# Kernel tuning notes

Measured on AMD Instinct MI355X. Metric: run time of the kernel, lower is better.

The kernel has to match this reference:

```python
import jax, jax.numpy as jnp
import numpy as np
import math

DIM = 768
HEADS = 12
HEAD_DIM = DIM // HEADS


def setup_inputs() -> dict:
    key = jax.random.key(0)
    ks = jax.random.split(key, 9)
    s = 1.0 / math.sqrt(DIM)
    x = jax.random.normal(ks[0], (8, 4096, DIM), dtype=jnp.float32)
    Wq = jax.random.normal(ks[1], (DIM, DIM), dtype=jnp.float32) * s
    bq = jnp.zeros((DIM,), dtype=jnp.float32)
    Wk = jax.random.normal(ks[2], (DIM, DIM), dtype=jnp.float32) * s
    bk = jnp.zeros((DIM,), dtype=jnp.float32)
    Wv = jax.random.normal(ks[3], (DIM, DIM), dtype=jnp.float32) * s
    bv = jnp.zeros((DIM,), dtype=jnp.float32)
    Wp = jax.random.normal(ks[4], (DIM, DIM), dtype=jnp.float32) * s
    bp = jnp.zeros((DIM,), dtype=jnp.float32)
    return {"x": x, "Wq": Wq, "bq": bq, "Wk": Wk, "bk": bk,
            "Wv": Wv, "bv": bv, "Wp": Wp, "bp": bp}


def reference(x, Wq, bq, Wk, bk, Wv, bv, Wp, bp):
    B, N, C = x.shape
    H, D = HEADS, HEAD_DIM
    # torch Linear: y = x @ W.T + b
    q = (x @ Wq.T + bq).reshape(B, N, H, D).transpose(0, 2, 1, 3)  # [B,H,N,D]
    k = (x @ Wk.T + bk).reshape(B, N, H, D).transpose(0, 2, 1, 3)
    v = (x @ Wv.T + bv).reshape(B, N, H, D).transpose(0, 2, 1, 3)
    q = jax.nn.softmax(q, axis=-1)   # softmax over head_dim
    k = jax.nn.softmax(k, axis=-2)   # softmax over sequence
    kv = jnp.einsum('bhnd,bhne->bhde', k, v) / math.sqrt(D)  # [B,H,D,D]
    out = jnp.einsum('bhnd,bhde->bhne', q, kv)               # [B,H,N,D]
    out = out.transpose(0, 2, 1, 3).reshape(B, N, C)
    return out @ Wp.T + bp
```

## Files before the change

kernel.cpp:

```cpp
#include <hip/hip_runtime.h>
#include <hip/hip_bf16.h>


#define AS1 __attribute__((address_space(1)))
#define AS3 __attribute__((address_space(3)))

typedef __attribute__((ext_vector_type(8))) short    s16x8;
typedef __attribute__((ext_vector_type(4))) float    f32x4;
typedef __attribute__((ext_vector_type(8))) _Float16 f16x8;
typedef __attribute__((ext_vector_type(4))) unsigned short u16x4;

__device__ __forceinline__ unsigned short f2bf(float f) {
  union { float f; unsigned u; } v; v.f = f;
  unsigned r = v.u + 0x7FFFu + ((v.u >> 16) & 1u);
  return (unsigned short)(r >> 16);
}

__global__ __launch_bounds__(256) void prep(const float* __restrict__ x,
                                            const float* __restrict__ Wq, const float* __restrict__ Wk,
                                            const float* __restrict__ Wv,
                                            const float* __restrict__ bq, const float* __restrict__ bk,
                                            const float* __restrict__ bv,
                                            unsigned short* __restrict__ x_bf,
                                            unsigned short* __restrict__ wqkv_bf,
                                            float* __restrict__ bqkv) {
  const int XB = 2304;
  if ((int)blockIdx.x >= XB) {
    int j = (blockIdx.x - XB) * 256 + threadIdx.x;
    if (j < 768) bqkv[j] = bq[j];
    else if (j < 1536) bqkv[j] = bk[j - 768];
    else if (j < 2304) bqkv[j] = bv[j - 1536];
    return;
  }
  const int n8x = 3145728, n8w = 73728;
  const int stride = XB * 256;
  for (int i = blockIdx.x * 256 + threadIdx.x; i < n8x + 3 * n8w; i += stride) {
    const float* s; unsigned short* d;
    if (i < n8x) { s = x + (size_t)i * 8; d = x_bf + (size_t)i * 8; }
    else {
      int wi = i - n8x, w = wi / n8w, off = wi - w * n8w;
      const float* ws_ = (w == 0) ? Wq : (w == 1) ? Wk : Wv;
      s = ws_ + (size_t)off * 8; d = wqkv_bf + (size_t)wi * 8;
    }
    f32x4 a = ((const f32x4*)s)[0], b = ((const f32x4*)s)[1];
    u16x4 lo, hi;
    lo[0] = f2bf(a[0]); lo[1] = f2bf(a[1]); lo[2] = f2bf(a[2]); lo[3] = f2bf(a[3]);
    hi[0] = f2bf(b[0]); hi[1] = f2bf(b[1]); hi[2] = f2bf(b[2]); hi[3] = f2bf(b[3]);
    ((u16x4*)d)[0] = lo; ((u16x4*)d)[1] = hi;
  }
}

template <int MODE, int BMBLK>
__global__ __launch_bounds__(512, 2) void gemm256(const unsigned short* __restrict__ A,
                                                  const unsigned short* __restrict__ Bm,
                                                  const float* __restrict__ bias,
                                                  void* out0, void* out1, void* out2,
                                                  int N, int K, int nb, int batchedB) {
  constexpr int BM = BMBLK * 128;
  __shared__ unsigned short As[2][BM * 64];
  __shared__ unsigned short Bs[2][256 * 64];
  const int tid = threadIdx.x, lane = tid & 63, wid = tid >> 6;
  const int wr = wid >> 2, wc = wid & 3;
  const int cpx = gridDim.x >> 3;
  const int logical = (blockIdx.x & 7) * cpx + (blockIdx.x >> 3);
  const int m0 = (logical / nb) * BM, n0 = (logical % nb) * 256;
  const unsigned short* Bp = Bm + (batchedB ? ((size_t)(m0 >> 12) * 589824) : 0);

  f32x4 acc[BMBLK * 4][4] = {};
  const int srcc8 = ((lane & 7) ^ (lane >> 3)) * 8;

  auto stageA = [&](int buf, int which, int k0) {
    if constexpr (BMBLK == 2) {
#pragma unroll
      for (int half = 0; half < 2; ++half) {
        int row = half * 128 + which * 64 + (tid >> 3);
        __builtin_amdgcn_global_load_lds(
            (const AS1 void*)(A + (size_t)(m0 + row) * K + k0 + srcc8),
            (AS3 void*)(&As[buf][row * 64 + (tid & 7) * 8]), 16, 0, 0);
      }
    } else {
#pragma unroll
      for (int j = 0; j < 2; ++j) {
        int row = j * 64 + (tid >> 3);
        __builtin_amdgcn_global_load_lds(
            (const AS1 void*)(A + (size_t)(m0 + row) * K + k0 + srcc8),
            (AS3 void*)(&As[buf][row * 64 + (tid & 7) * 8]), 16, 0, 0);
      }
    }
  };
  auto stageB = [&](int buf, int which, int k0) {
#pragma unroll
    for (int j = 0; j < 2; ++j) {
      int idx = tid + j * 512;
      int half = idx >> 9, sub = (idx >> 8) & 1;
      int row = half * 128 + sub * 64 + which * 32 + ((idx & 255) >> 3);
      __builtin_amdgcn_global_load_lds(
          (const AS1 void*)(Bp + (size_t)(n0 + row) * K + k0 + srcc8),
          (AS3 void*)(&Bs[buf][row * 64 + (idx & 7) * 8]), 16, 0, 0);
    }
  };

  const int r15 = lane & 15, hi8 = (lane >> 4) * 8, sw = (lane & 7) * 8;
  s16x8 af[4][2], bf[4][2];
  auto readA = [&](int buf, int grp) {
    const unsigned short* base = &As[buf][(wr * (BM / 2) + grp * 64) * 64];
#pragma unroll
    for (int i = 0; i < 4; ++i) {
      int lrow = i * 16 + r15;
#pragma unroll
      for (int kk = 0; kk < 2; ++kk)
        af[i][kk] = *(const s16x8*)(base + lrow * 64 + ((kk * 32 + hi8) ^ sw));
    }
  };
  auto readB = [&](int buf, int grp) {
    const unsigned short* base = &Bs[buf][(wc >> 1) * 128 * 64];
#pragma unroll
    for (int jj = 0; jj < 2; ++jj) {
      int j = grp * 2 + jj;
      int lrow = (wc & 1) * 64 + j * 16 + r15;
#pragma unroll
      for (int kk = 0; kk < 2; ++kk)
        bf[j][kk] = *(const s16x8*)(base + lrow * 64 + ((kk * 32 + hi8) ^ sw));
    }
  };

#define MFMA16(MI0, J0)                                                             \
  __builtin_amdgcn_s_setprio(1);                                                    \
  _Pragma("unroll") for (int kk = 0; kk < 2; ++kk)                                  \
  _Pragma("unroll") for (int i = 0; i < 4; ++i)                                     \
  _Pragma("unroll") for (int jj = 0; jj < 2; ++jj)                                  \
    acc[(MI0) + i][(J0) + jj] = __builtin_amdgcn_mfma_f32_16x16x32_bf16(            \
        af[i][kk], bf[(J0) + jj][kk], acc[(MI0) + i][(J0) + jj], 0, 0, 0);          \
  __builtin_amdgcn_s_setprio(0);

  const int nt = K >> 6;
  if constexpr (BMBLK == 2) {
    stageA(0, 0, 0);  stageA(0, 1, 0);  stageB(0, 0, 0);  stageB(0, 1, 0);
    stageA(1, 0, 64); stageA(1, 1, 64); stageB(1, 0, 64); stageB(1, 1, 64);
    asm volatile("s_waitcnt vmcnt(8)" ::: "memory");
  } else {
    stageA(0, 0, 0);  stageB(0, 0, 0);  stageB(0, 1, 0);
    stageA(1, 0, 64); stageB(1, 0, 64); stageB(1, 1, 64);
    asm volatile("s_waitcnt vmcnt(6)" ::: "memory");
  }
  __builtin_amdgcn_s_barrier();

  for (int s = 0; s < nt; ++s) {
    const int buf = s & 1;
    const int k2 = (s + 2) << 6;
    const bool pf = (s + 2) < nt;
    if constexpr (BMBLK == 2) {
      readA(buf, 0); readB(buf, 0);
      asm volatile("" ::: "memory");
      __builtin_amdgcn_s_barrier();
      asm volatile("s_waitcnt lgkmcnt(0)" ::: "memory");
      MFMA16(0, 0)
      asm volatile("" ::: "memory");
      __builtin_amdgcn_s_barrier();
      readB(buf, 1);
      if (pf) { stageA(buf, 0, k2); stageB(buf, 0, k2); }
      asm volatile("" ::: "memory");
      __builtin_amdgcn_s_barrier();
      asm volatile("s_waitcnt lgkmcnt(0)" ::: "memory");
      MFMA16(0, 2)
      asm volatile("" ::: "memory");
      __builtin_amdgcn_s_barrier();
      readA(buf, 1);
      if (pf) stageB(buf, 1, k2);
      asm volatile("" ::: "memory");
      __builtin_amdgcn_s_barrier();
      asm volatile("s_waitcnt lgkmcnt(0)" ::: "memory");
      MFMA16(4, 2)
      asm volatile("" ::: "memory");
      __builtin_amdgcn_s_barrier();
      if (pf) stageA(buf, 1, k2);
      MFMA16(4, 0)
      if (pf)              asm volatile("s_waitcnt vmcnt(8)" ::: "memory");
      else if (s + 1 < nt) asm volatile("s_waitcnt vmcnt(0)" ::: "memory");
      __builtin_amdgcn_s_barrier();
    } else {
      readA(buf, 0); readB(buf, 0); readB(buf, 1);
      asm volatile("" ::: "memory");
      __builtin_amdgcn_s_barrier();
      asm volatile("s_waitcnt lgkmcnt(0)" ::: "memory");
      MFMA16(0, 0)
      asm volatile("" ::: "memory");
      __builtin_amdgcn_s_barrier();
      if (pf) { stageA(buf, 0, k2); stageB(buf, 0, k2); stageB(buf, 1, k2); }
      MFMA16(0, 2)
      if (pf)              asm volatile("s_waitcnt vmcnt(6)" ::: "memory");
      else if (s + 1 < nt) asm volatile("s_waitcnt vmcnt(0)" ::: "memory");
      __builtin_amdgcn_s_barrier();
    }
  }

  const int g = lane >> 4, c15 = lane & 15;
  float bj[4];
#pragma unroll
  for (int j = 0; j < 4; ++j) bj[j] = bias[n0 + wc * 64 + j * 16 + c15];

  if (MODE == 0) {
    float* out = (float*)out0;
#pragma unroll
    for (int mi = 0; mi < BMBLK * 4; ++mi)
#pragma unroll
      for (int j = 0; j < 4; ++j) {
        int gr = m0 + wr * (BM / 2) + mi * 16 + g * 4;
        int gc = n0 + wc * 64 + j * 16 + c15;
#pragma unroll
        for (int r = 0; r < 4; ++r)
          out[(size_t)(gr + r) * N + gc] = acc[mi][j][r] + bj[j];
      }
  } else {
    if (n0 < 768) {
      unsigned short* qsm = (unsigned short*)out0;
      const int cbase = n0 + wc * 64;
#pragma unroll
      for (int mi = 0; mi < BMBLK * 4; ++mi) {
#pragma unroll
        for (int r = 0; r < 4; ++r) {
          int gr = m0 + wr * (BM / 2) + mi * 16 + g * 4 + r;
          float v[4];
#pragma unroll
          for (int j = 0; j < 4; ++j) v[j] = acc[mi][j][r] + bj[j];
          float mx = fmaxf(fmaxf(v[0], v[1]), fmaxf(v[2], v[3]));
#pragma unroll
          for (int st = 1; st < 16; st <<= 1) mx = fmaxf(mx, __shfl_xor(mx, st));
          float p[4], sm = 0.f;
#pragma unroll
          for (int j = 0; j < 4; ++j) { p[j] = __expf(v[j] - mx); sm += p[j]; }
#pragma unroll
          for (int st = 1; st < 16; st <<= 1) sm += __shfl_xor(sm, st);
          float inv = 1.0f / sm;
#pragma unroll
          for (int j = 0; j < 4; ++j)
            qsm[(size_t)gr * 768 + cbase + j * 16 + c15] = f2bf(p[j] * inv);
        }
      }
    } else {
      _Float16* dst = (n0 < 1536) ? (_Float16*)out1 : (_Float16*)out2;
      const int cbase = (n0 < 1536 ? n0 - 768 : n0 - 1536) + wc * 64;
#pragma unroll
      for (int mi = 0; mi < BMBLK * 4; ++mi)
#pragma unroll
        for (int j = 0; j < 4; ++j) {
          int gr = m0 + wr * (BM / 2) + mi * 16 + g * 4;
          int cc = cbase + j * 16 + c15;
#pragma unroll
          for (int r = 0; r < 4; ++r)
            dst[(size_t)(gr + r) * 768 + cc] = (_Float16)(acc[mi][j][r] + bj[j]);
        }
    }
  }
#undef MFMA16
}

__global__ __launch_bounds__(256) void kv_partial(const _Float16* __restrict__ kh,
                                                  const _Float16* __restrict__ vh,
                                                  float* __restrict__ kv_raw,
                                                  float* __restrict__ z_raw) {
  const int bh = blockIdx.x, b = bh / 12, h = bh % 12;
  const int split = blockIdx.y;
  __shared__ float ek_s[64][68];
  __shared__ float v_s[64][68];
  const int t = threadIdx.x;
  const int d0 = (t >> 4) * 4, e0 = (t & 15) * 4;
  const int zd = t & 63, zq = t >> 6;
  float acc[4][4] = {};
  float zp = 0.f;
  const size_t base = (size_t)b * 4096 * 768 + h * 64;

  for (int nc = 0; nc < 8; ++nc) {
    int n0 = split * 512 + nc * 64;
#pragma unroll
    for (int j = 0; j < 2; ++j) {
      int vi = t + j * 256;
      int row = vi >> 3, c8 = (vi & 7) * 8;
      size_t gp = base + (size_t)(n0 + row) * 768 + c8;
      f16x8 k8 = *(const f16x8*)(kh + gp);
      f16x8 v8 = *(const f16x8*)(vh + gp);
      f32x4 e0v, e1v, v0v, v1v;
#pragma unroll
      for (int u = 0; u < 4; ++u) {
        e0v[u] = __expf((float)k8[u]); e1v[u] = __expf((float)k8[4 + u]);
        v0v[u] = (float)v8[u];         v1v[u] = (float)v8[4 + u];
      }
      *(f32x4*)&ek_s[row][c8] = e0v; *(f32x4*)&ek_s[row][c8 + 4] = e1v;
      *(f32x4*)&v_s[row][c8]  = v0v; *(f32x4*)&v_s[row][c8 + 4]  = v1v;
    }
    __syncthreads();
#pragma unroll 4
    for (int r = 0; r < 16; ++r) zp += ek_s[zq * 16 + r][zd];
#pragma unroll 8
    for (int n = 0; n < 64; ++n) {
      f32x4 ekv = *(const f32x4*)&ek_s[n][d0];
      f32x4 vv  = *(const f32x4*)&v_s[n][e0];
#pragma unroll
      for (int i = 0; i < 4; ++i)
#pragma unroll
        for (int j = 0; j < 4; ++j)
          acc[i][j] += ekv[i] * vv[j];
    }
    __syncthreads();
  }
  float* kvp = kv_raw + (size_t)bh * 4096;
#pragma unroll
  for (int i = 0; i < 4; ++i)
#pragma unroll
    for (int j = 0; j < 4; ++j)
      atomicAdd(&kvp[(d0 + i) * 64 + e0 + j], acc[i][j]);
  atomicAdd(&z_raw[bh * 64 + zd], zp);
}

__global__ __launch_bounds__(256) void weff_build(const float* __restrict__ kv_raw,
                                                  const float* __restrict__ z_raw,
                                                  const float* __restrict__ Wp,
                                                  unsigned short* __restrict__ weffT) {
  const int c0 = blockIdx.x * 64, h = blockIdx.y, b = blockIdx.z;
  const int bh = b * 12 + h;
  __shared__ float kvn[64][65];
  const int t = threadIdx.x;
#pragma unroll
  for (int i = 0; i < 16; ++i) {
    int idx = t + i * 256;
    int d = idx >> 6;
    kvn[d][idx & 63] = kv_raw[(size_t)bh * 4096 + idx] / (z_raw[bh * 64 + d] * 8.0f);
  }
  __syncthreads();
  const int c = c0 + (t >> 2);
  const int d0 = (t & 3) * 16;
  const float* wrow = Wp + (size_t)c * 768 + h * 64;
  float acc[16] = {};
#pragma unroll 8
  for (int e = 0; e < 64; ++e) {
    float w = wrow[e];
#pragma unroll
    for (int dd = 0; dd < 16; ++dd) acc[dd] += w * kvn[d0 + dd][e];
  }
  unsigned short* orow = weffT + (size_t)b * 589824 + (size_t)c * 768 + h * 64 + d0;
#pragma unroll
  for (int dd = 0; dd < 16; ++dd) orow[dd] = f2bf(acc[dd]);
}

extern "C" void kernel_launch(void* const* d_in, const int* in_sizes, int n_in,
                              void* d_out, int out_size, void* d_ws, size_t ws_size,
                              hipStream_t stream) {
  const float* x  = (const float*)d_in[0];
  const float* Wq = (const float*)d_in[1];
  const float* bq = (const float*)d_in[2];
  const float* Wk = (const float*)d_in[3];
  const float* bk = (const float*)d_in[4];
  const float* Wv = (const float*)d_in[5];
  const float* bv = (const float*)d_in[6];
  const float* Wp = (const float*)d_in[7];
  const float* bp = (const float*)d_in[8];

  const size_t MT = 32768;
  const size_t XE = MT * 768;
  const size_t WE = 768 * 768;

  unsigned short* x_bf    = (unsigned short*)d_ws;
  unsigned short* wqkv_bf = x_bf + XE;
  unsigned short* q_sm    = wqkv_bf + 3 * WE;
  _Float16* k_h = (_Float16*)(q_sm + XE);
  _Float16* v_h = k_h + XE;
  unsigned short* weffT = (unsigned short*)(v_h + XE);
  float* bqkv   = (float*)(weffT + 8 * WE);
  float* kv_raw = bqkv + 2304;
  float* z_raw  = kv_raw + 96 * 4096;

  prep<<<2313, 256, 0, stream>>>(x, Wq, Wk, Wv, bq, bk, bv, x_bf, wqkv_bf, bqkv);
  hipMemsetAsync(kv_raw, 0, (96 * 4096 + 96 * 64) * sizeof(float), stream);

  gemm256<1, 2><<<1152, 512, 0, stream>>>(x_bf, wqkv_bf, bqkv, q_sm, k_h, v_h, 2304, 768, 9, 0);

  kv_partial<<<dim3(96, 8), 256, 0, stream>>>(k_h, v_h, kv_raw, z_raw);
  weff_build<<<dim3(12, 12, 8), 256, 0, stream>>>(kv_raw, z_raw, Wp, weffT);

  gemm256<0, 1><<<768, 512, 0, stream>>>(q_sm, weffT, bp, d_out, nullptr, nullptr, 768, 768, 3, 1);
}
```

Before: 356.3 us.

## Load GEMM B operand directly from global into registers, drop B LDS staging

The GEMM no longer stages the weight tile (B) through shared memory. Each wave instead loads its B fragments straight from global memory into registers every k-step, and only A keeps double-buffered LDS staging. The finely interleaved barrier/prefetch schedule is replaced by a simple loop: load B, prefetch next A, compute, then wait for all loads and barrier. This halves LDS use and removes the B LDS writes and reads. In exchange, B is fetched redundantly by the two wave rows, global loads now sit on the critical path with less overlap, and the full vmcnt(0) wait each iteration serializes memory and compute.

Result: slower. 456.0 us (+28.0%).

```diff
diff --git a/kernel.cpp b/kernel.cpp
--- a/kernel.cpp
+++ b/kernel.cpp
@@ -57,8 +57,9 @@
                                                   void* out0, void* out1, void* out2,
                                                   int N, int K, int nb, int batchedB) {
   constexpr int BM = BMBLK * 128;
+  constexpr int MI = BMBLK * 4;
+  constexpr int NSTG = 2 * BMBLK;
   __shared__ unsigned short As[2][BM * 64];
-  __shared__ unsigned short Bs[2][256 * 64];
   const int tid = threadIdx.x, lane = tid & 63, wid = tid >> 6;
   const int wr = wid >> 2, wc = wid & 3;
   const int cpx = gridDim.x >> 3;
@@ -66,132 +67,69 @@
   const int m0 = (logical / nb) * BM, n0 = (logical % nb) * 256;
   const unsigned short* Bp = Bm + (batchedB ? ((size_t)(m0 >> 12) * 589824) : 0);
 
-  f32x4 acc[BMBLK * 4][4] = {};
+  f32x4 acc[MI][4] = {};
   const int srcc8 = ((lane & 7) ^ (lane >> 3)) * 8;
-
-  auto stageA = [&](int buf, int which, int k0) {
-    if constexpr (BMBLK == 2) {
-#pragma unroll
-      for (int half = 0; half < 2; ++half) {
-        int row = half * 128 + which * 64 + (tid >> 3);
-        __builtin_amdgcn_global_load_lds(
-            (const AS1 void*)(A + (size_t)(m0 + row) * K + k0 + srcc8),
-            (AS3 void*)(&As[buf][row * 64 + (tid & 7) * 8]), 16, 0, 0);
-      }
-    } else {
-#pragma unroll
-      for (int j = 0; j < 2; ++j) {
-        int row = j * 64 + (tid >> 3);
-        __builtin_amdgcn_global_load_lds(
-            (const AS1 void*)(A + (size_t)(m0 + row) * K + k0 + srcc8),
-            (AS3 void*)(&As[buf][row * 64 + (tid & 7) * 8]), 16, 0, 0);
-      }
+  const int r15 = lane & 15, hi8 = (lane >> 4) * 8, sw = (lane & 7) * 8;
+
+  auto stageA = [&](int buf, int k0) {
+#pragma unroll
+    for (int j = 0; j < NSTG; ++j) {
+      int row = j * 64 + (tid >> 3);
+      __builtin_amdgcn_global_load_lds(
+          (const AS1 void*)(A + (size_t)(m0 + row) * K + k0 + srcc8),
+          (AS3 void*)(&As[buf][row * 64 + (tid & 7) * 8]), 16, 0, 0);
     }
   };
-  auto stageB = [&](int buf, int which, int k0) {
-#pragma unroll
-    for (int j = 0; j < 2; ++j) {
-      int idx = tid + j * 512;
-      int half = idx >> 9, sub = (idx >> 8) & 1;
-      int row = half * 128 + sub * 64 + which * 32 + ((idx & 255) >> 3);
-      __builtin_amdgcn_global_load_lds(
-          (const AS1 void*)(Bp + (size_t)(n0 + row) * K + k0 + srcc8),
-          (AS3 void*)(&Bs[buf][row * 64 + (idx & 7) * 8]), 16, 0, 0);
-    }
+
+  const unsigned short* Bw = Bp + (size_t)(n0 + wc * 64 + r15) * K + hi8;
+  s16x8 bf[4][2];
+  auto loadB = [&](int k0) {
+#pragma unroll
+    for (int j = 0; j < 4; ++j)
+#pragma unroll
+      for (int kk = 0; kk < 2; ++kk)
+        bf[j][kk] = *(const s16x8*)(Bw + (size_t)j * 16 * K + k0 + kk * 32);
   };
 
-  const int r15 = lane & 15, hi8 = (lane >> 4) * 8, sw = (lane & 7) * 8;
-  s16x8 af[4][2], bf[4][2];
+  s16x8 af[4][2];
   auto readA = [&](int buf, int grp) {
     const unsigned short* base = &As[buf][(wr * (BM / 2) + grp * 64) * 64];
 #pragma unroll
-    for (int i = 0; i < 4; ++i) {
-      int lrow = i * 16 + r15;
+    for (int i = 0; i < 4; ++i)
 #pragma unroll
       for (int kk = 0; kk < 2; ++kk)
-        af[i][kk] = *(const s16x8*)(base + lrow * 64 + ((kk * 32 + hi8) ^ sw));
-    }
+        af[i][kk] = *(const s16x8*)(base + (i * 16 + r15) * 64 + ((kk * 32 + hi8) ^ sw));
   };
-  auto readB = [&](int buf, int grp) {
-    const unsigned short* base = &Bs[buf][(wc >> 1) * 128 * 64];
-#pragma unroll
-    for (int jj = 0; jj < 2; ++jj) {
-      int j = grp * 2 + jj;
-      int lrow = (wc & 1) * 64 + j * 16 + r15;
-#pragma unroll
-      for (int kk = 0; kk < 2; ++kk)
-        bf[j][kk] = *(const s16x8*)(base + lrow * 64 + ((kk * 32 + hi8) ^ sw));
-    }
+  auto mfma32 = [&](int mi0) {
+    __builtin_amdgcn_s_setprio(1);
+#pragma unroll
+    for (int i = 0; i < 4; ++i)
+#pragma unroll
+      for (int j = 0; j < 4; ++j)
+#pragma unroll
+        for (int kk = 0; kk < 2; ++kk)
+          acc[mi0 + i][j] = __builtin_amdgcn_mfma_f32_16x16x32_bf16(
+              af[i][kk], bf[j][kk], acc[mi0 + i][j], 0, 0, 0);
+    __builtin_amdgcn_s_setprio(0);
   };
 
-#define MFMA16(MI0, J0)                                                             \
-  __builtin_amdgcn_s_setprio(1);                                                    \
-  _Pragma("unroll") for (int kk = 0; kk < 2; ++kk)                                  \
-  _Pragma("unroll") for (int i = 0; i < 4; ++i)                                     \
-  _Pragma("unroll") for (int jj = 0; jj < 2; ++jj)                                  \
-    acc[(MI0) + i][(J0) + jj] = __builtin_amdgcn_mfma_f32_16x16x32_bf16(            \
-        af[i][kk], bf[(J0) + jj][kk], acc[(MI0) + i][(J0) + jj], 0, 0, 0);          \
-  __builtin_amdgcn_s_setprio(0);
-
   const int nt = K >> 6;
-  if constexpr (BMBLK == 2) {
-    stageA(0, 0, 0);  stageA(0, 1, 0);  stageB(0, 0, 0);  stageB(0, 1, 0);
-    stageA(1, 0, 64); stageA(1, 1, 64); stageB(1, 0, 64); stageB(1, 1, 64);
-    asm volatile("s_waitcnt vmcnt(8)" ::: "memory");
-  } else {
-    stageA(0, 0, 0);  stageB(0, 0, 0);  stageB(0, 1, 0);
-    stageA(1, 0, 64); stageB(1, 0, 64); stageB(1, 1, 64);
-    asm volatile("s_waitcnt vmcnt(6)" ::: "memory");
-  }
+  stageA(0, 0);
+  asm volatile("s_waitcnt vmcnt(0)" ::: "memory");
   __builtin_amdgcn_s_barrier();
 
-  for (int s = 0; s < nt; ++s) {
-    const int buf = s & 1;
-    const int k2 = (s + 2) << 6;
-    const bool pf = (s + 2) < nt;
+  for (int t = 0; t < nt; ++t) {
+    const int buf = t & 1;
+    loadB(t << 6);
+    if (t + 1 < nt) stageA(buf ^ 1, (t + 1) << 6);
+    readA(buf, 0);
+    mfma32(0);
     if constexpr (BMBLK == 2) {
-      readA(buf, 0); readB(buf, 0);
-      asm volatile("" ::: "memory");
-      __builtin_amdgcn_s_barrier();
-      asm volatile("s_waitcnt lgkmcnt(0)" ::: "memory");
-      MFMA16(0, 0)
-      asm volatile("" ::: "memory");
-      __builtin_amdgcn_s_barrier();
-      readB(buf, 1);
-      if (pf) { stageA(buf, 0, k2); stageB(buf, 0, k2); }
-      asm volatile("" ::: "memory");
-      __builtin_amdgcn_s_barrier();
-      asm volatile("s_waitcnt lgkmcnt(0)" ::: "memory");
-      MFMA16(0, 2)
-      asm volatile("" ::: "memory");
-      __builtin_amdgcn_s_barrier();
       readA(buf, 1);
-      if (pf) stageB(buf, 1, k2);
-      asm volatile("" ::: "memory");
-      __builtin_amdgcn_s_barrier();
-      asm volatile("s_waitcnt lgkmcnt(0)" ::: "memory");
-      MFMA16(4, 2)
-      asm volatile("" ::: "memory");
-      __builtin_amdgcn_s_barrier();
-      if (pf) stageA(buf, 1, k2);
-      MFMA16(4, 0)
-      if (pf)              asm volatile("s_waitcnt vmcnt(8)" ::: "memory");
-      else if (s + 1 < nt) asm volatile("s_waitcnt vmcnt(0)" ::: "memory");
-      __builtin_amdgcn_s_barrier();
-    } else {
-      readA(buf, 0); readB(buf, 0); readB(buf, 1);
-      asm volatile("" ::: "memory");
-      __builtin_amdgcn_s_barrier();
-      asm volatile("s_waitcnt lgkmcnt(0)" ::: "memory");
-      MFMA16(0, 0)
-      asm volatile("" ::: "memory");
-      __builtin_amdgcn_s_barrier();
-      if (pf) { stageA(buf, 0, k2); stageB(buf, 0, k2); stageB(buf, 1, k2); }
-      MFMA16(0, 2)
-      if (pf)              asm volatile("s_waitcnt vmcnt(6)" ::: "memory");
-      else if (s + 1 < nt) asm volatile("s_waitcnt vmcnt(0)" ::: "memory");
-      __builtin_amdgcn_s_barrier();
-    }
+      mfma32(4);
+    }
+    asm volatile("s_waitcnt vmcnt(0)" ::: "memory");
+    __builtin_amdgcn_s_barrier();
   }
 
   const int g = lane >> 4, c15 = lane & 15;
@@ -202,7 +140,7 @@
   if (MODE == 0) {
     float* out = (float*)out0;
 #pragma unroll
-    for (int mi = 0; mi < BMBLK * 4; ++mi)
+    for (int mi = 0; mi < MI; ++mi)
 #pragma unroll
       for (int j = 0; j < 4; ++j) {
         int gr = m0 + wr * (BM / 2) + mi * 16 + g * 4;
@@ -216,7 +154,7 @@
       unsigned short* qsm = (unsigned short*)out0;
       const int cbase = n0 + wc * 64;
 #pragma unroll
-      for (int mi = 0; mi < BMBLK * 4; ++mi) {
+      for (int mi = 0; mi < MI; ++mi) {
 #pragma unroll
         for (int r = 0; r < 4; ++r) {
           int gr = m0 + wr * (BM / 2) + mi * 16 + g * 4 + r;
@@ -241,7 +179,7 @@
       _Float16* dst = (n0 < 1536) ? (_Float16*)out1 : (_Float16*)out2;
       const int cbase = (n0 < 1536 ? n0 - 768 : n0 - 1536) + wc * 64;
 #pragma unroll
-      for (int mi = 0; mi < BMBLK * 4; ++mi)
+      for (int mi = 0; mi < MI; ++mi)
 #pragma unroll
         for (int j = 0; j < 4; ++j) {
           int gr = m0 + wr * (BM / 2) + mi * 16 + g * 4;
@@ -252,7 +190,6 @@
         }
     }
   }
-#undef MFMA16
 }
 
 __global__ __launch_bounds__(256) void kv_partial(const _Float16* __restrict__ kh,
```

## Switch GEMM to 32x32x16 MFMA tiles and fold memset into prep kernel

Applied to the files above, without the earlier changes.

Changes both GEMM instantiations from 16x16x32 bf16 MFMA to 32x32x16 bf16 MFMA. Fragment loads, accumulator layout and all epilogues (bias, q softmax over 64 columns, fp16 stores) are rewritten for the new 32-row output mapping. The aim is fewer MFMA issues and LDS fragment reads per tile. It also drops the separate hipMemsetAsync and zeroes kv_raw/z_raw inside the tail blocks of the prep kernel, removing one launch. The softmax epilogue now shuffles across 32 lanes, and the strided per-element stores may hurt coalescing.

New measurement: 381.5 us. +7.1%, slower.

```diff
diff --git a/kernel.cpp b/kernel.cpp
--- a/kernel.cpp
+++ b/kernel.cpp
@@ -7,7 +7,9 @@
 
 typedef __attribute__((ext_vector_type(8))) short    s16x8;
 typedef __attribute__((ext_vector_type(4))) float    f32x4;
+typedef __attribute__((ext_vector_type(16))) float   f32x16;
 typedef __attribute__((ext_vector_type(8))) _Float16 f16x8;
+typedef __attribute__((ext_vector_type(4))) _Float16 f16x4;
 typedef __attribute__((ext_vector_type(4))) unsigned short u16x4;
 
 __device__ __forceinline__ unsigned short f2bf(float f) {
@@ -23,13 +25,16 @@
                                             const float* __restrict__ bv,
                                             unsigned short* __restrict__ x_bf,
                                             unsigned short* __restrict__ wqkv_bf,
-                                            float* __restrict__ bqkv) {
+                                            float* __restrict__ bqkv,
+                                            float* __restrict__ kvz) {
   const int XB = 2304;
   if ((int)blockIdx.x >= XB) {
     int j = (blockIdx.x - XB) * 256 + threadIdx.x;
     if (j < 768) bqkv[j] = bq[j];
     else if (j < 1536) bqkv[j] = bk[j - 768];
     else if (j < 2304) bqkv[j] = bv[j - 1536];
+    const int NZ = 96 * 4096 + 96 * 64;
+    for (int i = (blockIdx.x - XB) * 256 + threadIdx.x; i < NZ; i += 9 * 256) kvz[i] = 0.f;
     return;
   }
   const int n8x = 3145728, n8w = 73728;
@@ -56,7 +61,9 @@
                                                   const float* __restrict__ bias,
                                                   void* out0, void* out1, void* out2,
                                                   int N, int K, int nb, int batchedB) {
-  constexpr int BM = BMBLK * 128;
+  constexpr int BM  = BMBLK * 128;
+  constexpr int MIH = BMBLK;
+  constexpr int MIF = BMBLK * 2;
   __shared__ unsigned short As[2][BM * 64];
   __shared__ unsigned short Bs[2][256 * 64];
   const int tid = threadIdx.x, lane = tid & 63, wid = tid >> 6;
@@ -66,8 +73,9 @@
   const int m0 = (logical / nb) * BM, n0 = (logical % nb) * 256;
   const unsigned short* Bp = Bm + (batchedB ? ((size_t)(m0 >> 12) * 589824) : 0);
 
-  f32x4 acc[BMBLK * 4][4] = {};
+  f32x16 acc[MIF][2] = {};
   const int srcc8 = ((lane & 7) ^ (lane >> 3)) * 8;
+  const int l31 = lane & 31, g8 = (lane >> 5) * 8, sw = (lane & 7) * 8;
 
   auto stageA = [&](int buf, int which, int k0) {
     if constexpr (BMBLK == 2) {
@@ -100,38 +108,33 @@
     }
   };
 
-  const int r15 = lane & 15, hi8 = (lane >> 4) * 8, sw = (lane & 7) * 8;
-  s16x8 af[4][2], bf[4][2];
-  auto readA = [&](int buf, int grp) {
-    const unsigned short* base = &As[buf][(wr * (BM / 2) + grp * 64) * 64];
-#pragma unroll
-    for (int i = 0; i < 4; ++i) {
-      int lrow = i * 16 + r15;
-#pragma unroll
-      for (int kk = 0; kk < 2; ++kk)
-        af[i][kk] = *(const s16x8*)(base + lrow * 64 + ((kk * 32 + hi8) ^ sw));
-    }
-  };
-  auto readB = [&](int buf, int grp) {
+  s16x8 af[2][4], bf[2][4];
+  auto readA = [&](int buf, int h) {
+    const unsigned short* base = &As[buf][(wr * (BM / 2) + h * (BM / 4)) * 64];
+#pragma unroll
+    for (int i = 0; i < MIH; ++i)
+#pragma unroll
+      for (int ks = 0; ks < 4; ++ks)
+        af[BMBLK == 2 ? i : h][ks] =
+            *(const s16x8*)(base + (i * 32 + l31) * 64 + ((ks * 16 + g8) ^ sw));
+  };
+  auto readB = [&](int buf, int q) {
     const unsigned short* base = &Bs[buf][(wc >> 1) * 128 * 64];
-#pragma unroll
-    for (int jj = 0; jj < 2; ++jj) {
-      int j = grp * 2 + jj;
-      int lrow = (wc & 1) * 64 + j * 16 + r15;
-#pragma unroll
-      for (int kk = 0; kk < 2; ++kk)
-        bf[j][kk] = *(const s16x8*)(base + lrow * 64 + ((kk * 32 + hi8) ^ sw));
-    }
-  };
-
-#define MFMA16(MI0, J0)                                                             \
-  __builtin_amdgcn_s_setprio(1);                                                    \
-  _Pragma("unroll") for (int kk = 0; kk < 2; ++kk)                                  \
-  _Pragma("unroll") for (int i = 0; i < 4; ++i)                                     \
-  _Pragma("unroll") for (int jj = 0; jj < 2; ++jj)                                  \
-    acc[(MI0) + i][(J0) + jj] = __builtin_amdgcn_mfma_f32_16x16x32_bf16(            \
-        af[i][kk], bf[(J0) + jj][kk], acc[(MI0) + i][(J0) + jj], 0, 0, 0);          \
-  __builtin_amdgcn_s_setprio(0);
+    int lrow = (wc & 1) * 64 + q * 32 + l31;
+#pragma unroll
+    for (int ks = 0; ks < 4; ++ks)
+      bf[q][ks] = *(const s16x8*)(base + lrow * 64 + ((ks * 16 + g8) ^ sw));
+  };
+  auto mfmaQ = [&](int h, int q) {
+    __builtin_amdgcn_s_setprio(1);
+#pragma unroll
+    for (int ks = 0; ks < 4; ++ks)
+#pragma unroll
+      for (int i = 0; i < MIH; ++i)
+        acc[h * MIH + i][q] = __builtin_amdgcn_mfma_f32_32x32x16_bf16(
+            af[BMBLK == 2 ? i : h][ks], bf[q][ks], acc[h * MIH + i][q], 0, 0, 0);
+    __builtin_amdgcn_s_setprio(0);
+  };
 
   const int nt = K >> 6;
   if constexpr (BMBLK == 2) {
@@ -154,7 +157,7 @@
       asm volatile("" ::: "memory");
       __builtin_amdgcn_s_barrier();
       asm volatile("s_waitcnt lgkmcnt(0)" ::: "memory");
-      MFMA16(0, 0)
+      mfmaQ(0, 0);
       asm volatile("" ::: "memory");
       __builtin_amdgcn_s_barrier();
       readB(buf, 1);
@@ -162,7 +165,7 @@
       asm volatile("" ::: "memory");
       __builtin_amdgcn_s_barrier();
       asm volatile("s_waitcnt lgkmcnt(0)" ::: "memory");
-      MFMA16(0, 2)
+      mfmaQ(0, 1);
       asm volatile("" ::: "memory");
       __builtin_amdgcn_s_barrier();
       readA(buf, 1);
@@ -170,89 +173,90 @@
       asm volatile("" ::: "memory");
       __builtin_amdgcn_s_barrier();
       asm volatile("s_waitcnt lgkmcnt(0)" ::: "memory");
-      MFMA16(4, 2)
+      mfmaQ(1, 1);
       asm volatile("" ::: "memory");
       __builtin_amdgcn_s_barrier();
       if (pf) stageA(buf, 1, k2);
-      MFMA16(4, 0)
+      mfmaQ(1, 0);
       if (pf)              asm volatile("s_waitcnt vmcnt(8)" ::: "memory");
       else if (s + 1 < nt) asm volatile("s_waitcnt vmcnt(0)" ::: "memory");
       __builtin_amdgcn_s_barrier();
     } else {
-      readA(buf, 0); readB(buf, 0); readB(buf, 1);
+      readA(buf, 0); readA(buf, 1); readB(buf, 0); readB(buf, 1);
       asm volatile("" ::: "memory");
       __builtin_amdgcn_s_barrier();
       asm volatile("s_waitcnt lgkmcnt(0)" ::: "memory");
-      MFMA16(0, 0)
+      mfmaQ(0, 0); mfmaQ(1, 0);
       asm volatile("" ::: "memory");
       __builtin_amdgcn_s_barrier();
       if (pf) { stageA(buf, 0, k2); stageB(buf, 0, k2); stageB(buf, 1, k2); }
-      MFMA16(0, 2)
+      mfmaQ(0, 1); mfmaQ(1, 1);
       if (pf)              asm volatile("s_waitcnt vmcnt(6)" ::: "memory");
       else if (s + 1 < nt) asm volatile("s_waitcnt vmcnt(0)" ::: "memory");
       __builtin_amdgcn_s_barrier();
     }
   }
 
-  const int g = lane >> 4, c15 = lane & 15;
-  float bj[4];
-#pragma unroll
-  for (int j = 0; j < 4; ++j) bj[j] = bias[n0 + wc * 64 + j * 16 + c15];
+  const int grp = lane >> 5;
+  float bj[2];
+#pragma unroll
+  for (int q = 0; q < 2; ++q) bj[q] = bias[n0 + wc * 64 + q * 32 + l31];
 
   if (MODE == 0) {
     float* out = (float*)out0;
 #pragma unroll
-    for (int mi = 0; mi < BMBLK * 4; ++mi)
-#pragma unroll
-      for (int j = 0; j < 4; ++j) {
-        int gr = m0 + wr * (BM / 2) + mi * 16 + g * 4;
-        int gc = n0 + wc * 64 + j * 16 + c15;
-#pragma unroll
-        for (int r = 0; r < 4; ++r)
-          out[(size_t)(gr + r) * N + gc] = acc[mi][j][r] + bj[j];
+    for (int mi = 0; mi < MIF; ++mi)
+#pragma unroll
+      for (int q = 0; q < 2; ++q) {
+        int gc = n0 + wc * 64 + q * 32 + l31;
+#pragma unroll
+        for (int r = 0; r < 16; ++r) {
+          int rr = (r & 3) + 8 * (r >> 2) + 4 * grp;
+          int gr = m0 + wr * (BM / 2) + mi * 32 + rr;
+          out[(size_t)gr * N + gc] = acc[mi][q][r] + bj[q];
+        }
       }
   } else {
     if (n0 < 768) {
       unsigned short* qsm = (unsigned short*)out0;
       const int cbase = n0 + wc * 64;
 #pragma unroll
-      for (int mi = 0; mi < BMBLK * 4; ++mi) {
-#pragma unroll
-        for (int r = 0; r < 4; ++r) {
-          int gr = m0 + wr * (BM / 2) + mi * 16 + g * 4 + r;
-          float v[4];
-#pragma unroll
-          for (int j = 0; j < 4; ++j) v[j] = acc[mi][j][r] + bj[j];
-          float mx = fmaxf(fmaxf(v[0], v[1]), fmaxf(v[2], v[3]));
-#pragma unroll
-          for (int st = 1; st < 16; st <<= 1) mx = fmaxf(mx, __shfl_xor(mx, st));
-          float p[4], sm = 0.f;
-#pragma unroll
-          for (int j = 0; j < 4; ++j) { p[j] = __expf(v[j] - mx); sm += p[j]; }
-#pragma unroll
-          for (int st = 1; st < 16; st <<= 1) sm += __shfl_xor(sm, st);
+      for (int mi = 0; mi < MIF; ++mi) {
+#pragma unroll
+        for (int r = 0; r < 16; ++r) {
+          int rr = (r & 3) + 8 * (r >> 2) + 4 * grp;
+          int gr = m0 + wr * (BM / 2) + mi * 32 + rr;
+          float v0 = acc[mi][0][r] + bj[0];
+          float v1 = acc[mi][1][r] + bj[1];
+          float mx = fmaxf(v0, v1);
+#pragma unroll
+          for (int st = 1; st < 32; st <<= 1) mx = fmaxf(mx, __shfl_xor(mx, st));
+          float p0 = __expf(v0 - mx), p1 = __expf(v1 - mx);
+          float sm = p0 + p1;
+#pragma unroll
+          for (int st = 1; st < 32; st <<= 1) sm += __shfl_xor(sm, st);
           float inv = 1.0f / sm;
-#pragma unroll
-          for (int j = 0; j < 4; ++j)
-            qsm[(size_t)gr * 768 + cbase + j * 16 + c15] = f2bf(p[j] * inv);
+          qsm[(size_t)gr * 768 + cbase + l31]      = f2bf(p0 * inv);
+          qsm[(size_t)gr * 768 + cbase + 32 + l31] = f2bf(p1 * inv);
         }
       }
     } else {
       _Float16* dst = (n0 < 1536) ? (_Float16*)out1 : (_Float16*)out2;
       const int cbase = (n0 < 1536 ? n0 - 768 : n0 - 1536) + wc * 64;
 #pragma unroll
-      for (int mi = 0; mi < BMBLK * 4; ++mi)
-#pragma unroll
-        for (int j = 0; j < 4; ++j) {
-          int gr = m0 + wr * (BM / 2) + mi * 16 + g * 4;
-          int cc = cbase + j * 16 + c15;
-#pragma unroll
-          for (int r = 0; r < 4; ++r)
-            dst[(size_t)(gr + r) * 768 + cc] = (_Float16)(acc[mi][j][r] + bj[j]);
+      for (int mi = 0; mi < MIF; ++mi)
+#pragma unroll
+        for (int q = 0; q < 2; ++q) {
+          int cc = cbase + q * 32 + l31;
+#pragma unroll
+          for (int r = 0; r < 16; ++r) {
+            int rr = (r & 3) + 8 * (r >> 2) + 4 * grp;
+            int gr = m0 + wr * (BM / 2) + mi * 32 + rr;
+            dst[(size_t)gr * 768 + cc] = (_Float16)(acc[mi][q][r] + bj[q]);
+          }
         }
     }
   }
-#undef MFMA16
 }
 
 __global__ __launch_bounds__(256) void kv_partial(const _Float16* __restrict__ kh,
@@ -369,8 +373,7 @@
   float* kv_raw = bqkv + 2304;
   float* z_raw  = kv_raw + 96 * 4096;
 
-  prep<<<2313, 256, 0, stream>>>(x, Wq, Wk, Wv, bq, bk, bv, x_bf, wqkv_bf, bqkv);
-  hipMemsetAsync(kv_raw, 0, (96 * 4096 + 96 * 64) * sizeof(float), stream);
+  prep<<<2313, 256, 0, stream>>>(x, Wq, Wk, Wv, bq, bk, bv, x_bf, wqkv_bf, bqkv, kv_raw);
 
   gemm256<1, 2><<<1152, 512, 0, stream>>>(x_bf, wqkv_bf, bqkv, q_sm, k_h, v_h, 2304, 768, 9, 0);
 
```
